# Performance work log

Measured on AMD Instinct MI355X. Metric: run time of the kernel, lower is better.

The kernel has to match this reference:

```python
import jax, jax.numpy as jnp
import numpy as np

N = 10000
E = 160000
IN_DIM = 256
PROJ_DIM = 512
HIDDEN = 512
OUT_DIM = 512
HEADS1, HEADS2, HEADS3 = 4, 4, 1
NEG_SLOPE = 0.2  # PyG GATConv default


def gat_conv(x, edge_index, W, att_src, att_dst, bias, heads, out_c, concat):
    """PyG GATConv (eval mode), with self-loops already appended to edge_index.
    x: [N, F_in]; W: [F_in, heads*out_c]; att_src/att_dst: [heads, out_c]; bias: [heads*out_c] or [out_c]."""
    n = x.shape[0]
    h = (x @ W).reshape(n, heads, out_c)            # [N, H, C]
    a_src = jnp.einsum('nhc,hc->nh', h, att_src)     # [N, H]
    a_dst = jnp.einsum('nhc,hc->nh', h, att_dst)     # [N, H]
    src, dst = edge_index[0], edge_index[1]
    e = jax.nn.leaky_relu(a_src[src] + a_dst[dst], NEG_SLOPE)  # [E, H]
    # segment softmax over incoming edges per destination node
    e_max = jax.ops.segment_max(e, dst, num_segments=n)
    e_exp = jnp.exp(e - e_max[dst])
    denom = jax.ops.segment_sum(e_exp, dst, num_segments=n)
    alpha = e_exp / denom[dst]                       # [E, H]
    msg = alpha[:, :, None] * h[src]                 # [E, H, C]
    out = jax.ops.segment_sum(msg, dst, num_segments=n)  # [N, H, C]
    out = out.reshape(n, heads * out_c) if concat else out.mean(axis=1)
    return out + bias


def setup_inputs() -> dict:
    key = jax.random.key(0)
    ks = jax.random.split(key, 16)
    g = 0.1
    inp = {
        'x': jax.random.normal(ks[0], (N, IN_DIM), dtype=jnp.float32),
        'edge_index': jax.random.randint(ks[1], (2, E), 0, N, dtype=jnp.int64),
        'proj_W': jax.random.normal(ks[2], (IN_DIM, PROJ_DIM), dtype=jnp.float32) * g,
        'proj_b': jnp.zeros((PROJ_DIM,), dtype=jnp.float32),
        'W1': jax.random.normal(ks[3], (PROJ_DIM, HEADS1 * HIDDEN), dtype=jnp.float32) * g,
        'as1': jax.random.normal(ks[4], (HEADS1, HIDDEN), dtype=jnp.float32) * g,
        'ad1': jax.random.normal(ks[5], (HEADS1, HIDDEN), dtype=jnp.float32) * g,
        'b1': jnp.zeros((HEADS1 * HIDDEN,), dtype=jnp.float32),
        'W2': jax.random.normal(ks[6], (HEADS1 * HIDDEN, HEADS2 * HIDDEN), dtype=jnp.float32) * g * 0.5,
        'as2': jax.random.normal(ks[7], (HEADS2, HIDDEN), dtype=jnp.float32) * g,
        'ad2': jax.random.normal(ks[8], (HEADS2, HIDDEN), dtype=jnp.float32) * g,
        'b2': jnp.zeros((HEADS2 * HIDDEN,), dtype=jnp.float32),
        'W3': jax.random.normal(ks[9], (HEADS2 * HIDDEN, HEADS3 * OUT_DIM), dtype=jnp.float32) * g * 0.5,
        'as3': jax.random.normal(ks[10], (HEADS3, OUT_DIM), dtype=jnp.float32) * g,
        'ad3': jax.random.normal(ks[11], (HEADS3, OUT_DIM), dtype=jnp.float32) * g,
        'b3': jnp.zeros((OUT_DIM,), dtype=jnp.float32),
    }
    return inp


def reference(x, edge_index, proj_W, proj_b, W1, as1, ad1, b1, W2, as2, ad2, b2, W3, as3, ad3, b3):
    # append self-loops once (PyG GATConv add_self_loops=True)
    loops = jnp.arange(N, dtype=edge_index.dtype)
    ei = jnp.concatenate([edge_index, jnp.stack([loops, loops])], axis=1)
    h = x @ proj_W + proj_b                                   # [N, 512]
    h = jax.nn.elu(gat_conv(h, ei, W1, as1, ad1, b1, HEADS1, HIDDEN, True))
    h = jax.nn.elu(gat_conv(h, ei, W2, as2, ad2, b2, HEADS2, HIDDEN, True))
    return gat_conv(h, ei, W3, as3, ad3, b3, HEADS3, OUT_DIM, False)  # [N, 512]
```

## Files before the change

### kernel.cpp

```cpp
#include <hip/hip_runtime.h>
#include <hip/hip_bf16.h>


#define LB(x) __launch_bounds__(x)

typedef unsigned short u16;
typedef unsigned int u32;
typedef __attribute__((ext_vector_type(8))) short short8;
typedef __attribute__((ext_vector_type(8))) short bf16x8;
typedef __attribute__((ext_vector_type(8))) _Float16 f16x8;
typedef __attribute__((ext_vector_type(4))) float f32x4;

__device__ __forceinline__ float b2f(u16 u) {
    union { float f; u32 u; } x;
    x.u = ((u32)u) << 16;
    return x.f;
}
__device__ __forceinline__ u16 f2b(float f) {
    u32 u = __float_as_uint(f);
    u = (u + 0x7FFFu + ((u >> 16) & 1u)) >> 16;
    return (u16)u;
}
__device__ __forceinline__ u16 f2h(float f) {
    union { _Float16 h; u16 u; } x;
    x.h = (_Float16)f;
    return x.u;
}
__device__ __forceinline__ float h2f(u16 u) {
    union { _Float16 h; u16 u; } x;
    x.u = u;
    return (float)x.h;
}
__device__ __forceinline__ void lds_cp16(const void* g, void* l) {
    __builtin_amdgcn_global_load_lds(
        (const __attribute__((address_space(1))) unsigned int*)g,
        (__attribute__((address_space(3))) unsigned int*)l, 16, 0, 0);
}

__global__ void k_deg(const int* __restrict__ ei, int E, int Np, int* __restrict__ deg) {
    int e = blockIdx.x * blockDim.x + threadIdx.x;
    if (e >= E + Np) return;
    int dst = (e < E) ? ei[E + e] : (e - E);
    atomicAdd(&deg[dst], 1);
}

__global__ LB(256) void k_s1(const int* __restrict__ deg, int* __restrict__ row_ptr,
                             int* __restrict__ bsum, int n) {
    __shared__ int sh[256];
    int b = blockIdx.x, t = threadIdx.x;
    int i = b * 256 + t;
    int v = (i < n) ? deg[i] : 0;
    sh[t] = v;
    __syncthreads();
    #pragma unroll
    for (int off = 1; off < 256; off <<= 1) {
        int add = (t >= off) ? sh[t - off] : 0;
        __syncthreads();
        sh[t] += add;
        __syncthreads();
    }
    if (i < n) row_ptr[i + 1] = sh[t];
    if (t == 255) bsum[b] = sh[255];
}

__global__ LB(64) void k_s2(int* __restrict__ bsum, int* __restrict__ boff, int nb) {
    __shared__ int sh[64];
    int t = threadIdx.x;
    sh[t] = (t < nb) ? bsum[t] : 0;
    __syncthreads();
    #pragma unroll
    for (int off = 1; off < 64; off <<= 1) {
        int add = (t >= off) ? sh[t - off] : 0;
        __syncthreads();
        sh[t] += add;
        __syncthreads();
    }
    if (t < nb) boff[t] = (t == 0) ? 0 : sh[t - 1];
}

__global__ LB(256) void k_s3(const int* __restrict__ deg, int* __restrict__ row_ptr,
                             const int* __restrict__ boff, int* __restrict__ cursor, int n) {
    int b = blockIdx.x, t = threadIdx.x;
    int i = b * 256 + t;
    if (i == 0) row_ptr[0] = 0;
    if (i < n) {
        int inc = row_ptr[i + 1] + boff[b];
        row_ptr[i + 1] = inc;
        cursor[i] = inc - deg[i];
    }
}

__global__ void k_fill(const int* __restrict__ ei, int E, int Np,
                       int* __restrict__ cursor, int* __restrict__ col_src) {
    int e = blockIdx.x * blockDim.x + threadIdx.x;
    if (e >= E + Np) return;
    int src, dst;
    if (e < E) { src = ei[e]; dst = ei[E + e]; }
    else       { src = dst = e - E; }
    int pos = atomicAdd(&cursor[dst], 1);
    col_src[pos] = src;
}

__global__ void k_pack(const float* __restrict__ in, u16* __restrict__ hi,
                       u16* __restrict__ lo, int n4) {
    int i = blockIdx.x * blockDim.x + threadIdx.x;
    if (i >= n4) return;
    float4 v = ((const float4*)in)[i];
    ushort4 h, l;
    h.x = f2b(v.x); l.x = f2b(v.x - b2f(h.x));
    h.y = f2b(v.y); l.y = f2b(v.y - b2f(h.y));
    h.z = f2b(v.z); l.z = f2b(v.z - b2f(h.z));
    h.w = f2b(v.w); l.w = f2b(v.w - b2f(h.w));
    ((ushort4*)hi)[i] = h;
    ((ushort4*)lo)[i] = l;
}

template<bool F16S>
__global__ LB(256) void k_wt_pack(const float* __restrict__ W, u16* __restrict__ Whi,
                                  u16* __restrict__ Wlo, int K, int Nn) {
    __shared__ float sh[32][33];
    int n0 = blockIdx.x * 32, k0 = blockIdx.y * 32;
    int c = threadIdx.x & 31, r0 = threadIdx.x >> 5;
    #pragma unroll
    for (int r = r0; r < 32; r += 8)
        sh[r][c] = W[(size_t)(k0 + r) * Nn + n0 + c];
    __syncthreads();
    #pragma unroll
    for (int r = r0; r < 32; r += 8) {
        float v = sh[c][r];
        if (F16S) {
            Whi[(size_t)(n0 + r) * K + k0 + c] = f2h(v);
        } else {
            u16 hi = f2b(v);
            Whi[(size_t)(n0 + r) * K + k0 + c] = hi;
            Wlo[(size_t)(n0 + r) * K + k0 + c] = f2b(v - b2f(hi));
        }
    }
}

__global__ LB(64) void k_bfold(const float* __restrict__ pb,
                               const u16* __restrict__ w1t_hi, const u16* __restrict__ w1t_lo,
                               float* __restrict__ bfold, int K) {
    int n = blockIdx.x;
    int lane = threadIdx.x;
    float s = 0.f;
    for (int k = lane; k < K; k += 64) {
        float w = b2f(w1t_hi[(size_t)n * K + k]) + b2f(w1t_lo[(size_t)n * K + k]);
        s = fmaf(pb[k], w, s);
    }
    #pragma unroll
    for (int off = 32; off; off >>= 1) s += __shfl_xor(s, off);
    if (lane == 0) bfold[n] = s;
}

template<int NFR, int PREC, int OUTMODE, bool ATT>
__global__ LB(256) void k_gemm_pl(const u16* __restrict__ Ahi, const u16* __restrict__ Alo,
                                  const u16* __restrict__ Bhi, const u16* __restrict__ Blo,
                                  const float* __restrict__ bias,
                                  u16* __restrict__ Chi, u16* __restrict__ Clo,
                                  u16* __restrict__ Cf16,
                                  const float* __restrict__ att_s, const float* __restrict__ att_d,
                                  float* __restrict__ a_src, float* __restrict__ a_dst,
                                  int HH, int M, int K, int Nn) {
    constexpr int BN = NFR * 32;
    constexpr int ALO_SZ = (PREC == 0) ? 128 * 32 : 8;
    constexpr int BLO_SZ = (PREC == 0) ? BN * 32 : 8;
    __shared__ u16 AsHi[128 * 32];
    __shared__ u16 AsLo[ALO_SZ];
    __shared__ u16 BsHi[BN * 32];
    __shared__ u16 BsLo[BLO_SZ];
    const int tid  = threadIdx.x;
    const int lane = tid & 63;
    const int w    = tid >> 6;
    const int wr   = w >> 1;
    const int wc   = w & 1;
    const int row0 = blockIdx.y * 128;
    const int col0 = blockIdx.x * BN;
    const int ln15 = lane & 15;
    const int lq   = lane >> 4;

    f32x4 acc[4][NFR];
    #pragma unroll
    for (int m = 0; m < 4; ++m)
        #pragma unroll
        for (int n = 0; n < NFR; ++n) acc[m][n] = (f32x4){0.f, 0.f, 0.f, 0.f};

    for (int k0 = 0; k0 < K; k0 += 32) {
        #pragma unroll
        for (int i = 0; i < 2; ++i) {
            int c = i * 256 + tid;
            int r  = 2 * (c >> 3) + (((c >> 2) ^ (c >> 4)) & 1);
            int kc = (c & 3) ^ (r & 3);
            int gra = row0 + r; if (gra >= M) gra = M - 1;
            size_t ga = (size_t)gra * K + k0 + kc * 8;
            lds_cp16(Ahi + ga, (char*)AsHi + c * 16);
            if (PREC == 0) lds_cp16(Alo + ga, (char*)AsLo + c * 16);
        }
        #pragma unroll
        for (int i = 0; i < NFR / 2; ++i) {
            int c = i * 256 + tid;
            int r  = 2 * (c >> 3) + (((c >> 2) ^ (c >> 4)) & 1);
            int kc = (c & 3) ^ (r & 3);
            size_t gb = (size_t)(col0 + r) * K + k0 + kc * 8;
            lds_cp16(Bhi + gb, (char*)BsHi + c * 16);
            if (PREC == 0) lds_cp16(Blo + gb, (char*)BsLo + c * 16);
        }
        __syncthreads();
        if (PREC == 0) {
            bf16x8 ah[4], al[4], bh[NFR], bl[NFR];
            #pragma unroll
            for (int m = 0; m < 4; ++m) {
                int row = wr * 64 + m * 16 + ln15;
                int byo = (row * 64 + lq * 16) ^ ((row & 7) << 4);
                ah[m] = *(const bf16x8*)((const char*)AsHi + byo);
                al[m] = *(const bf16x8*)((const char*)AsLo + byo);
            }
            #pragma unroll
            for (int n = 0; n < NFR; ++n) {
                int row = wc * (NFR * 16) + n * 16 + ln15;
                int byo = (row * 64 + lq * 16) ^ ((row & 7) << 4);
                bh[n] = *(const bf16x8*)((const char*)BsHi + byo);
                bl[n] = *(const bf16x8*)((const char*)BsLo + byo);
            }
            #pragma unroll
            for (int m = 0; m < 4; ++m)
                #pragma unroll
                for (int n = 0; n < NFR; ++n) {
                    acc[m][n] = __builtin_amdgcn_mfma_f32_16x16x32_bf16(al[m], bh[n], acc[m][n], 0, 0, 0);
                    acc[m][n] = __builtin_amdgcn_mfma_f32_16x16x32_bf16(ah[m], bl[n], acc[m][n], 0, 0, 0);
                    acc[m][n] = __builtin_amdgcn_mfma_f32_16x16x32_bf16(ah[m], bh[n], acc[m][n], 0, 0, 0);
                }
        } else {
            f16x8 a[4], b[NFR];
            #pragma unroll
            for (int m = 0; m < 4; ++m) {
                int row = wr * 64 + m * 16 + ln15;
                int byo = (row * 64 + lq * 16) ^ ((row & 7) << 4);
                a[m] = *(const f16x8*)((const char*)AsHi + byo);
            }
            #pragma unroll
            for (int n = 0; n < NFR; ++n) {
                int row = wc * (NFR * 16) + n * 16 + ln15;
                int byo = (row * 64 + lq * 16) ^ ((row & 7) << 4);
                b[n] = *(const f16x8*)((const char*)BsHi + byo);
            }
            #pragma unroll
            for (int m = 0; m < 4; ++m)
                #pragma unroll
                for (int n = 0; n < NFR; ++n)
                    acc[m][n] = __builtin_amdgcn_mfma_f32_16x16x32_f16(a[m], b[n], acc[m][n], 0, 0, 0);
        }
        __syncthreads();
    }

    #pragma unroll
    for (int m = 0; m < 4; ++m) {
        #pragma unroll
        for (int n = 0; n < NFR; ++n) {
            int gc = col0 + wc * (NFR * 16) + n * 16 + ln15;
            float badd = bias ? bias[gc] : 0.f;
            #pragma unroll
            for (int j = 0; j < 4; ++j) {
                int gr = row0 + wr * 64 + m * 16 + lq * 4 + j;
                if (gr < M) {
                    float v = acc[m][n][j] + badd;
                    size_t o = (size_t)gr * Nn + gc;
                    if (OUTMODE == 0) {
                        u16 hi = f2b(v);
                        Chi[o] = hi;
                        Clo[o] = f2b(v - b2f(hi));
                    } else {
                        Cf16[o] = f2h(v);
                    }
                }
            }
        }
    }

    if (ATT) {
        float atts[NFR], attd[NFR], bb[NFR];
        #pragma unroll
        for (int n = 0; n < NFR; ++n) {
            int gc = col0 + wc * (NFR * 16) + n * 16 + ln15;
            atts[n] = att_s[gc];
            attd[n] = att_d[gc];
            bb[n]   = bias ? bias[gc] : 0.f;
        }
        const int head = (col0 + wc * (NFR * 16)) >> 9;
        #pragma unroll
        for (int m = 0; m < 4; ++m) {
            #pragma unroll
            for (int j = 0; j < 4; ++j) {
                int gr = row0 + wr * 64 + m * 16 + lq * 4 + j;
                float s1 = 0.f, s2 = 0.f;
                #pragma unroll
                for (int n = 0; n < NFR; ++n) {
                    float v = acc[m][n][j] + bb[n];
                    s1 = fmaf(v, atts[n], s1);
                    s2 = fmaf(v, attd[n], s2);
                }
                #pragma unroll
                for (int off = 1; off < 16; off <<= 1) {
                    s1 += __shfl_xor(s1, off);
                    s2 += __shfl_xor(s2, off);
                }
                if (ln15 == 0 && gr < M) {
                    atomicAdd(&a_src[gr * HH + head], s1);
                    atomicAdd(&a_dst[gr * HH + head], s2);
                }
            }
        }
    }
}

template<int HH>
__global__ LB(64) void k_softmax(const int* __restrict__ row_ptr, const int* __restrict__ col_src,
                                 const float* __restrict__ a_src, const float* __restrict__ a_dst,
                                 float* __restrict__ alpha) {
    int d = blockIdx.x;
    int t = threadIdx.x;
    int s = row_ptr[d], eend = row_ptr[d + 1];
    int cnt = eend - s;
    float adh[HH];
    #pragma unroll
    for (int h = 0; h < HH; ++h) adh[h] = a_dst[d * HH + h];

    if (cnt <= 64) {
        bool act = t < cnt;
        float av[HH];
        #pragma unroll
        for (int h = 0; h < HH; ++h) av[h] = 0.f;
        if (act) {
            int src = col_src[s + t];
            if (HH == 4) {
                float4 q = ((const float4*)a_src)[src];
                av[0] = q.x; av[1] = q.y; av[2] = q.z; av[3] = q.w;
            } else {
                av[0] = a_src[src];
            }
        }
        float v[HH], m[HH], sum[HH];
        #pragma unroll
        for (int h = 0; h < HH; ++h) {
            float x = av[h] + adh[h];
            x = (x > 0.f) ? x : 0.2f * x;
            v[h] = act ? x : -1e30f;
            m[h] = v[h];
        }
        #pragma unroll
        for (int off = 32; off; off >>= 1)
            #pragma unroll
            for (int h = 0; h < HH; ++h) m[h] = fmaxf(m[h], __shfl_xor(m[h], off));
        #pragma unroll
        for (int h = 0; h < HH; ++h) {
            float e = act ? __expf(v[h] - m[h]) : 0.f;
            v[h] = e;
            sum[h] = e;
        }
        #pragma unroll
        for (int off = 32; off; off >>= 1)
            #pragma unroll
            for (int h = 0; h < HH; ++h) sum[h] += __shfl_xor(sum[h], off);
        if (act) {
            if (HH == 4) {
                float4 o;
                o.x = v[0] / sum[0]; o.y = v[1] / sum[1];
                o.z = v[2] / sum[2]; o.w = v[3] / sum[3];
                ((float4*)alpha)[s + t] = o;
            } else {
                alpha[s + t] = v[0] / sum[0];
            }
        }
        return;
    }

    for (int h = 0; h < HH; ++h) {
        float m = -1e30f;
        for (int e = s + t; e < eend; e += 64) {
            float x = a_src[col_src[e] * HH + h] + adh[h];
            x = (x > 0.f) ? x : 0.2f * x;
            m = fmaxf(m, x);
        }
        #pragma unroll
        for (int off = 32; off; off >>= 1) m = fmaxf(m, __shfl_xor(m, off));
        float sum = 0.f;
        for (int e = s + t; e < eend; e += 64) {
            float x = a_src[col_src[e] * HH + h] + adh[h];
            x = (x > 0.f) ? x : 0.2f * x;
            sum += __expf(x - m);
        }
        #pragma unroll
        for (int off = 32; off; off >>= 1) sum += __shfl_xor(sum, off);
        float inv = 1.0f / sum;
        for (int e = s + t; e < eend; e += 64) {
            float x = a_src[col_src[e] * HH + h] + adh[h];
            x = (x > 0.f) ? x : 0.2f * x;
            alpha[e * HH + h] = __expf(x - m) * inv;
        }
    }
}

template <int OMODE, bool ELU_>
__global__ LB(256) void k_agg(const int* __restrict__ row_ptr, const int* __restrict__ col_src,
                              const float* __restrict__ alpha, const u16* __restrict__ hf,
                              const float* __restrict__ bias,
                              u16* __restrict__ Oh, float* __restrict__ Of, int H, int C) {
    int d = blockIdx.x;
    int tid = threadIdx.x;
    int F = H * C;
    int o = tid * 8;
    int h0 = o / C;
    float acc[8];
    #pragma unroll
    for (int j = 0; j < 8; ++j) acc[j] = 0.f;
    int s = row_ptr[d], eend = row_ptr[d + 1];

    short8 v; float a;
    if (s < eend) {
        int src = col_src[s];
        a = alpha[s * H + h0];
        v = *(const short8*)(hf + (size_t)src * F + o);
    }
    for (int e = s; e < eend; ++e) {
        short8 w_; float an;
        bool more = (e + 1 < eend);
        if (more) {
            int srcn = col_src[e + 1];
            an = alpha[(e + 1) * H + h0];
            w_ = *(const short8*)(hf + (size_t)srcn * F + o);
        }
        #pragma unroll
        for (int j = 0; j < 8; ++j)
            acc[j] = fmaf(a, h2f((u16)v[j]), acc[j]);
        if (more) { a = an; v = w_; }
    }

    #pragma unroll
    for (int j = 0; j < 8; ++j) {
        acc[j] += bias[o + j];
        if (ELU_) acc[j] = (acc[j] > 0.f) ? acc[j] : __expf(acc[j]) - 1.f;
    }
    if (OMODE == 0) {
        short8 r;
        #pragma unroll
        for (int j = 0; j < 8; ++j) r[j] = (short)f2h(acc[j]);
        *(short8*)(Oh + (size_t)d * F + o) = r;
    } else {
        float* po = Of + (size_t)d * F + o;
        #pragma unroll
        for (int j4 = 0; j4 < 2; ++j4) {
            float4 r;
            r.x = acc[j4 * 4 + 0]; r.y = acc[j4 * 4 + 1];
            r.z = acc[j4 * 4 + 2]; r.w = acc[j4 * 4 + 3];
            *(float4*)&po[j4 * 4] = r;
        }
    }
}

extern "C" void kernel_launch(void* const* d_in, const int* in_sizes, int n_in,
                              void* d_out, int out_size, void* d_ws, size_t ws_size,
                              hipStream_t stream) {
    const float* x      = (const float*)d_in[0];
    const int*   ei     = (const int*)d_in[1];
    const float* proj_W = (const float*)d_in[2];
    const float* proj_b = (const float*)d_in[3];
    const float* W1  = (const float*)d_in[4];
    const float* as1 = (const float*)d_in[5];
    const float* ad1 = (const float*)d_in[6];
    const float* b1  = (const float*)d_in[7];
    const float* W2  = (const float*)d_in[8];
    const float* as2 = (const float*)d_in[9];
    const float* ad2 = (const float*)d_in[10];
    const float* b2  = (const float*)d_in[11];
    const float* W3  = (const float*)d_in[12];
    const float* as3 = (const float*)d_in[13];
    const float* ad3 = (const float*)d_in[14];
    const float* b3  = (const float*)d_in[15];

    const int N  = in_sizes[0] / 256;
    const int E  = in_sizes[1] / 2;
    const int Ep = E + N;
    const int NB = (N + 255) / 256;

    size_t off = 0;
    auto alloc = [&](size_t bytes) -> void* {
        void* p = (char*)d_ws + off;
        off += (bytes + 255) & ~(size_t)255;
        return p;
    };
    u16* bufX    = (u16*)alloc((size_t)N * 2048 * 2);
    u16* bufY    = (u16*)alloc((size_t)N * 2048 * 2);
    u16* xb_hi   = (u16*)alloc((size_t)N * 256 * 2);
    u16* xb_lo   = (u16*)alloc((size_t)N * 256 * 2);
    u16* pw_hi   = (u16*)alloc((size_t)256 * 512 * 2);
    u16* pw_lo   = (u16*)alloc((size_t)256 * 512 * 2);
    u16* wf_hi   = (u16*)alloc((size_t)2048 * 256 * 2);
    u16* wf_lo   = (u16*)alloc((size_t)2048 * 256 * 2);
    float* bfold   = (float*)alloc((size_t)2048 * 4);
    float* att_z   = (float*)alloc((size_t)N * 18 * 4);
    float* alpha   = (float*)alloc((size_t)Ep * 4 * 4);
    int*   deg     = (int*)alloc((size_t)N * 4);
    int*   cursor  = (int*)alloc((size_t)N * 4);
    int*   row_ptr = (int*)alloc((size_t)(N + 1) * 4);
    int*   col_src = (int*)alloc((size_t)Ep * 4);
    int*   bsum    = (int*)alloc((size_t)NB * 4);
    int*   boff    = (int*)alloc((size_t)NB * 4);
    (void)ws_size;

    float* a_src1 = att_z;
    float* a_dst1 = att_z + (size_t)N * 4;
    float* a_src2 = att_z + (size_t)N * 8;
    float* a_dst2 = att_z + (size_t)N * 12;
    float* a_src3 = att_z + (size_t)N * 16;
    float* a_dst3 = att_z + (size_t)N * 17;

    u16* whi = (u16*)d_out;
    u16* wlo = (u16*)d_out + (size_t)2048 * 2048;

    hipMemsetAsync(deg, 0, (size_t)N * 4, stream);
    hipMemsetAsync(att_z, 0, (size_t)N * 18 * 4, stream);
    int eb = (Ep + 255) / 256;
    k_deg<<<eb, 256, 0, stream>>>(ei, E, N, deg);
    k_s1<<<NB, 256, 0, stream>>>(deg, row_ptr, bsum, N);
    k_s2<<<1, 64, 0, stream>>>(bsum, boff, NB);
    k_s3<<<NB, 256, 0, stream>>>(deg, row_ptr, boff, cursor, N);
    k_fill<<<eb, 256, 0, stream>>>(ei, E, N, cursor, col_src);

    const int MB1 = (N + 127) / 128;

    k_pack<<<(N * 256 / 4 + 255) / 256, 256, 0, stream>>>(x, xb_hi, xb_lo, N * 256 / 4);
    k_pack<<<(256 * 512 / 4 + 255) / 256, 256, 0, stream>>>(proj_W, pw_hi, pw_lo, 256 * 512 / 4);

    k_wt_pack<false><<<dim3(2048 / 32, 512 / 32), 256, 0, stream>>>(W1, whi, wlo, 512, 2048);
    k_bfold<<<2048, 64, 0, stream>>>(proj_b, whi, wlo, bfold, 512);
    k_gemm_pl<2, 0, 0, false><<<dim3(256 / 64, 2048 / 128), 256, 0, stream>>>(
        whi, wlo, pw_hi, pw_lo, nullptr, wf_hi, wf_lo, nullptr,
        nullptr, nullptr, nullptr, nullptr, 0, 2048, 512, 256);

    k_gemm_pl<4, 0, 2, true><<<dim3(2048 / 128, MB1), 256, 0, stream>>>(
        xb_hi, xb_lo, wf_hi, wf_lo, bfold, nullptr, nullptr, bufX,
        as1, ad1, a_src1, a_dst1, 4, N, 256, 2048);
    k_softmax<4><<<N, 64, 0, stream>>>(row_ptr, col_src, a_src1, a_dst1, alpha);
    k_agg<0, true><<<N, 256, 0, stream>>>(row_ptr, col_src, alpha, bufX,
                                          b1, bufY, nullptr, 4, 512);

    k_wt_pack<true><<<dim3(2048 / 32, 2048 / 32), 256, 0, stream>>>(W2, whi, nullptr, 2048, 2048);
    k_gemm_pl<4, 2, 2, true><<<dim3(2048 / 128, MB1), 256, 0, stream>>>(
        bufY, nullptr, whi, nullptr, nullptr, nullptr, nullptr, bufX,
        as2, ad2, a_src2, a_dst2, 4, N, 2048, 2048);
    k_softmax<4><<<N, 64, 0, stream>>>(row_ptr, col_src, a_src2, a_dst2, alpha);
    k_agg<0, true><<<N, 256, 0, stream>>>(row_ptr, col_src, alpha, bufX,
                                          b2, bufY, nullptr, 4, 512);

    k_wt_pack<true><<<dim3(512 / 32, 2048 / 32), 256, 0, stream>>>(W3, whi, nullptr, 2048, 512);
    k_gemm_pl<2, 2, 2, true><<<dim3(512 / 64, MB1), 256, 0, stream>>>(
        bufY, nullptr, whi, nullptr, nullptr, nullptr, nullptr, bufX,
        as3, ad3, a_src3, a_dst3, 1, N, 2048, 512);
    k_softmax<1><<<N, 64, 0, stream>>>(row_ptr, col_src, a_src3, a_dst3, alpha);
    k_agg<1, false><<<N, 64, 0, stream>>>(row_ptr, col_src, alpha, bufX,
                                          b3, nullptr, (float*)d_out, 1, 512);
}
```

Before: 638.0 us.

## Fuse segment softmax into aggregation and widen layer-2 GEMM tile to 256 rows

Merges the per-destination softmax kernel into the aggregation kernel. Each wavefront now computes attention weights for its own head into shared memory and consumes them directly, so the alpha buffer and one launch per layer go away. The GEMM is templated on warp rows so the large layer-2 GEMM can use 512-thread, 256-row tiles to improve B-tile reuse. Risks are extra block syncs in the high-degree path, a larger LDS footprint, and a loader indexing scheme that must still cover the larger tiles correctly.

```diff
diff --git a/kernel.cpp b/kernel.cpp
--- a/kernel.cpp
+++ b/kernel.cpp
@@ -153,19 +153,23 @@
     if (lane == 0) bfold[n] = s;
 }
 
-template<int NFR, int PREC, int OUTMODE, bool ATT>
-__global__ LB(256) void k_gemm_pl(const u16* __restrict__ Ahi, const u16* __restrict__ Alo,
-                                  const u16* __restrict__ Bhi, const u16* __restrict__ Blo,
-                                  const float* __restrict__ bias,
-                                  u16* __restrict__ Chi, u16* __restrict__ Clo,
-                                  u16* __restrict__ Cf16,
-                                  const float* __restrict__ att_s, const float* __restrict__ att_d,
-                                  float* __restrict__ a_src, float* __restrict__ a_dst,
-                                  int HH, int M, int K, int Nn) {
+template<int WM, int NFR, int PREC, int OUTMODE, bool ATT>
+__global__ __launch_bounds__(WM * 128)
+void k_gemm_pl(const u16* __restrict__ Ahi, const u16* __restrict__ Alo,
+               const u16* __restrict__ Bhi, const u16* __restrict__ Blo,
+               const float* __restrict__ bias,
+               u16* __restrict__ Chi, u16* __restrict__ Clo,
+               u16* __restrict__ Cf16,
+               const float* __restrict__ att_s, const float* __restrict__ att_d,
+               float* __restrict__ a_src, float* __restrict__ a_dst,
+               int HH, int M, int K, int Nn) {
+    constexpr int BM = WM * 64;
     constexpr int BN = NFR * 32;
-    constexpr int ALO_SZ = (PREC == 0) ? 128 * 32 : 8;
+    constexpr int T  = WM * 128;
+    constexpr int BITER = (NFR * 128) / T > 0 ? (NFR * 128) / T : 1;
+    constexpr int ALO_SZ = (PREC == 0) ? BM * 32 : 8;
     constexpr int BLO_SZ = (PREC == 0) ? BN * 32 : 8;
-    __shared__ u16 AsHi[128 * 32];
+    __shared__ u16 AsHi[BM * 32];
     __shared__ u16 AsLo[ALO_SZ];
     __shared__ u16 BsHi[BN * 32];
     __shared__ u16 BsLo[BLO_SZ];
@@ -174,7 +178,7 @@
     const int w    = tid >> 6;
     const int wr   = w >> 1;
     const int wc   = w & 1;
-    const int row0 = blockIdx.y * 128;
+    const int row0 = blockIdx.y * BM;
     const int col0 = blockIdx.x * BN;
     const int ln15 = lane & 15;
     const int lq   = lane >> 4;
@@ -188,7 +192,7 @@
     for (int k0 = 0; k0 < K; k0 += 32) {
         #pragma unroll
         for (int i = 0; i < 2; ++i) {
-            int c = i * 256 + tid;
+            int c = i * T + tid;
             int r  = 2 * (c >> 3) + (((c >> 2) ^ (c >> 4)) & 1);
             int kc = (c & 3) ^ (r & 3);
             int gra = row0 + r; if (gra >= M) gra = M - 1;
@@ -197,8 +201,8 @@
             if (PREC == 0) lds_cp16(Alo + ga, (char*)AsLo + c * 16);
         }
         #pragma unroll
-        for (int i = 0; i < NFR / 2; ++i) {
-            int c = i * 256 + tid;
+        for (int i = 0; i < BITER; ++i) {
+            int c = i * T + tid;
             int r  = 2 * (c >> 3) + (((c >> 2) ^ (c >> 4)) & 1);
             int kc = (c & 3) ^ (r & 3);
             size_t gb = (size_t)(col0 + r) * K + k0 + kc * 8;
@@ -313,126 +317,101 @@
     }
 }
 
-template<int HH>
-__global__ LB(64) void k_softmax(const int* __restrict__ row_ptr, const int* __restrict__ col_src,
-                                 const float* __restrict__ a_src, const float* __restrict__ a_dst,
-                                 float* __restrict__ alpha) {
-    int d = blockIdx.x;
-    int t = threadIdx.x;
-    int s = row_ptr[d], eend = row_ptr[d + 1];
-    int cnt = eend - s;
-    float adh[HH];
-    #pragma unroll
-    for (int h = 0; h < HH; ++h) adh[h] = a_dst[d * HH + h];
+template <int HH, int OMODE, bool ELU_>
+__global__ __launch_bounds__(HH * 64)
+void k_sagg(const int* __restrict__ row_ptr, const int* __restrict__ col_src,
+            const float* __restrict__ a_src, const float* __restrict__ a_dst,
+            const u16* __restrict__ hf, const float* __restrict__ bias,
+            u16* __restrict__ Oh, float* __restrict__ Of, int C) {
+    __shared__ float sal[HH * 64];
+    const int d    = blockIdx.x;
+    const int tid  = threadIdx.x;
+    const int w    = tid >> 6;
+    const int lane = tid & 63;
+    const int F    = HH * C;
+    const int o    = tid * 8;
+    const int s = row_ptr[d], eend = row_ptr[d + 1];
+    const int cnt = eend - s;
+    const float adh = a_dst[d * HH + w];
+
+    float acc[8];
+    #pragma unroll
+    for (int j = 0; j < 8; ++j) acc[j] = 0.f;
 
     if (cnt <= 64) {
-        bool act = t < cnt;
-        float av[HH];
-        #pragma unroll
-        for (int h = 0; h < HH; ++h) av[h] = 0.f;
-        if (act) {
-            int src = col_src[s + t];
-            if (HH == 4) {
-                float4 q = ((const float4*)a_src)[src];
-                av[0] = q.x; av[1] = q.y; av[2] = q.z; av[3] = q.w;
-            } else {
-                av[0] = a_src[src];
-            }
-        }
-        float v[HH], m[HH], sum[HH];
-        #pragma unroll
-        for (int h = 0; h < HH; ++h) {
-            float x = av[h] + adh[h];
-            x = (x > 0.f) ? x : 0.2f * x;
-            v[h] = act ? x : -1e30f;
-            m[h] = v[h];
-        }
-        #pragma unroll
-        for (int off = 32; off; off >>= 1)
-            #pragma unroll
-            for (int h = 0; h < HH; ++h) m[h] = fmaxf(m[h], __shfl_xor(m[h], off));
-        #pragma unroll
-        for (int h = 0; h < HH; ++h) {
-            float e = act ? __expf(v[h] - m[h]) : 0.f;
-            v[h] = e;
-            sum[h] = e;
-        }
-        #pragma unroll
-        for (int off = 32; off; off >>= 1)
-            #pragma unroll
-            for (int h = 0; h < HH; ++h) sum[h] += __shfl_xor(sum[h], off);
-        if (act) {
-            if (HH == 4) {
-                float4 o;
-                o.x = v[0] / sum[0]; o.y = v[1] / sum[1];
-                o.z = v[2] / sum[2]; o.w = v[3] / sum[3];
-                ((float4*)alpha)[s + t] = o;
-            } else {
-                alpha[s + t] = v[0] / sum[0];
-            }
-        }
-        return;
-    }
-
-    for (int h = 0; h < HH; ++h) {
+        bool act = lane < cnt;
+        float av = act ? a_src[col_src[s + lane] * HH + w] : 0.f;
+        float x = av + adh;
+        x = (x > 0.f) ? x : 0.2f * x;
+        float v = act ? x : -1e30f;
+        float m = v;
+        #pragma unroll
+        for (int off = 32; off; off >>= 1) m = fmaxf(m, __shfl_xor(m, off));
+        float e_ = act ? __expf(v - m) : 0.f;
+        float sum = e_;
+        #pragma unroll
+        for (int off = 32; off; off >>= 1) sum += __shfl_xor(sum, off);
+        if (act) sal[w * 64 + lane] = e_ / sum;
+        __syncthreads();
+
+        if (cnt > 0) {
+            short8 vv; float a;
+            {
+                int src0 = col_src[s];
+                a = sal[w * 64];
+                vv = *(const short8*)(hf + (size_t)src0 * F + o);
+            }
+            for (int i = 0; i < cnt; ++i) {
+                short8 w_; float an;
+                bool more = (i + 1 < cnt);
+                if (more) {
+                    int srcn = col_src[s + i + 1];
+                    an = sal[w * 64 + i + 1];
+                    w_ = *(const short8*)(hf + (size_t)srcn * F + o);
+                }
+                #pragma unroll
+                for (int j = 0; j < 8; ++j)
+                    acc[j] = fmaf(a, h2f((u16)vv[j]), acc[j]);
+                if (more) { a = an; vv = w_; }
+            }
+        }
+    } else {
         float m = -1e30f;
-        for (int e = s + t; e < eend; e += 64) {
-            float x = a_src[col_src[e] * HH + h] + adh[h];
+        for (int e = s + lane; e < eend; e += 64) {
+            float x = a_src[col_src[e] * HH + w] + adh;
             x = (x > 0.f) ? x : 0.2f * x;
             m = fmaxf(m, x);
         }
         #pragma unroll
         for (int off = 32; off; off >>= 1) m = fmaxf(m, __shfl_xor(m, off));
         float sum = 0.f;
-        for (int e = s + t; e < eend; e += 64) {
-            float x = a_src[col_src[e] * HH + h] + adh[h];
+        for (int e = s + lane; e < eend; e += 64) {
+            float x = a_src[col_src[e] * HH + w] + adh;
             x = (x > 0.f) ? x : 0.2f * x;
             sum += __expf(x - m);
         }
         #pragma unroll
         for (int off = 32; off; off >>= 1) sum += __shfl_xor(sum, off);
         float inv = 1.0f / sum;
-        for (int e = s + t; e < eend; e += 64) {
-            float x = a_src[col_src[e] * HH + h] + adh[h];
-            x = (x > 0.f) ? x : 0.2f * x;
-            alpha[e * HH + h] = __expf(x - m) * inv;
-        }
-    }
-}
-
-template <int OMODE, bool ELU_>
-__global__ LB(256) void k_agg(const int* __restrict__ row_ptr, const int* __restrict__ col_src,
-                              const float* __restrict__ alpha, const u16* __restrict__ hf,
-                              const float* __restrict__ bias,
-                              u16* __restrict__ Oh, float* __restrict__ Of, int H, int C) {
-    int d = blockIdx.x;
-    int tid = threadIdx.x;
-    int F = H * C;
-    int o = tid * 8;
-    int h0 = o / C;
-    float acc[8];
-    #pragma unroll
-    for (int j = 0; j < 8; ++j) acc[j] = 0.f;
-    int s = row_ptr[d], eend = row_ptr[d + 1];
-
-    short8 v; float a;
-    if (s < eend) {
-        int src = col_src[s];
-        a = alpha[s * H + h0];
-        v = *(const short8*)(hf + (size_t)src * F + o);
-    }
-    for (int e = s; e < eend; ++e) {
-        short8 w_; float an;
-        bool more = (e + 1 < eend);
-        if (more) {
-            int srcn = col_src[e + 1];
-            an = alpha[(e + 1) * H + h0];
-            w_ = *(const short8*)(hf + (size_t)srcn * F + o);
-        }
-        #pragma unroll
-        for (int j = 0; j < 8; ++j)
-            acc[j] = fmaf(a, h2f((u16)v[j]), acc[j]);
-        if (more) { a = an; v = w_; }
+        for (int base = s; base < eend; base += 64) {
+            int e = base + lane;
+            if (e < eend) {
+                float x = a_src[col_src[e] * HH + w] + adh;
+                x = (x > 0.f) ? x : 0.2f * x;
+                sal[w * 64 + lane] = __expf(x - m) * inv;
+            }
+            __syncthreads();
+            int nn = (eend - base < 64) ? (eend - base) : 64;
+            for (int i = 0; i < nn; ++i) {
+                int src = col_src[base + i];
+                float a = sal[w * 64 + i];
+                short8 vv = *(const short8*)(hf + (size_t)src * F + o);
+                #pragma unroll
+                for (int j = 0; j < 8; ++j)
+                    acc[j] = fmaf(a, h2f((u16)vv[j]), acc[j]);
+            }
+            __syncthreads();
+        }
     }
 
     #pragma unroll
@@ -498,7 +477,6 @@
     u16* wf_lo   = (u16*)alloc((size_t)2048 * 256 * 2);
     float* bfold   = (float*)alloc((size_t)2048 * 4);
     float* att_z   = (float*)alloc((size_t)N * 18 * 4);
-    float* alpha   = (float*)alloc((size_t)Ep * 4 * 4);
     int*   deg     = (int*)alloc((size_t)N * 4);
     int*   cursor  = (int*)alloc((size_t)N * 4);
     int*   row_ptr = (int*)alloc((size_t)(N + 1) * 4);
@@ -527,36 +505,34 @@
     k_fill<<<eb, 256, 0, stream>>>(ei, E, N, cursor, col_src);
 
     const int MB1 = (N + 127) / 128;
+    const int MB2 = (N + 255) / 256;
 
     k_pack<<<(N * 256 / 4 + 255) / 256, 256, 0, stream>>>(x, xb_hi, xb_lo, N * 256 / 4);
     k_pack<<<(256 * 512 / 4 + 255) / 256, 256, 0, stream>>>(proj_W, pw_hi, pw_lo, 256 * 512 / 4);
 
     k_wt_pack<false><<<dim3(2048 / 32, 512 / 32), 256, 0, stream>>>(W1, whi, wlo, 512, 2048);
     k_bfold<<<2048, 64, 0, stream>>>(proj_b, whi, wlo, bfold, 512);
-    k_gemm_pl<2, 0, 0, false><<<dim3(256 / 64, 2048 / 128), 256, 0, stream>>>(
+    k_gemm_pl<2, 2, 0, 0, false><<<dim3(256 / 64, 2048 / 128), 256, 0, stream>>>(
         whi, wlo, pw_hi, pw_lo, nullptr, wf_hi, wf_lo, nullptr,
         nullptr, nullptr, nullptr, nullptr, 0, 2048, 512, 256);
 
-    k_gemm_pl<4, 0, 2, true><<<dim3(2048 / 128, MB1), 256, 0, stream>>>(
+    k_gemm_pl<2, 4, 0, 2, true><<<dim3(2048 / 128, MB1), 256, 0, stream>>>(
         xb_hi, xb_lo, wf_hi, wf_lo, bfold, nullptr, nullptr, bufX,
         as1, ad1, a_src1, a_dst1, 4, N, 256, 2048);
-    k_softmax<4><<<N, 64, 0, stream>>>(row_ptr, col_src, a_src1, a_dst1, alpha);
-    k_agg<0, true><<<N, 256, 0, stream>>>(row_ptr, col_src, alpha, bufX,
-                                          b1, bufY, nullptr, 4, 512);
+    k_sagg<4, 0, true><<<N, 256, 0, stream>>>(row_ptr, col_src, a_src1, a_dst1,
+                                              bufX, b1, bufY, nullptr, 512);
 
     k_wt_pack<true><<<dim3(2048 / 32, 2048 / 32), 256, 0, stream>>>(W2, whi, nullptr, 2048, 2048);
-    k_gemm_pl<4, 2, 2, true><<<dim3(2048 / 128, MB1), 256, 0, stream>>>(
+    k_gemm_pl<4, 4, 2, 2, true><<<dim3(2048 / 128, MB2), 512, 0, stream>>>(
         bufY, nullptr, whi, nullptr, nullptr, nullptr, nullptr, bufX,
         as2, ad2, a_src2, a_dst2, 4, N, 2048, 2048);
-    k_softmax<4><<<N, 64, 0, stream>>>(row_ptr, col_src, a_src2, a_dst2, alpha);
-    k_agg<0, true><<<N, 256, 0, stream>>>(row_ptr, col_src, alpha, bufX,
-                                          b2, bufY, nullptr, 4, 512);
+    k_sagg<4, 0, true><<<N, 256, 0, stream>>>(row_ptr, col_src, a_src2, a_dst2,
+                                              bufX, b2, bufY, nullptr, 512);
 
     k_wt_pack<true><<<dim3(512 / 32, 2048 / 32), 256, 0, stream>>>(W3, whi, nullptr, 2048, 512);
-    k_gemm_pl<2, 2, 2, true><<<dim3(512 / 64, MB1), 256, 0, stream>>>(
+    k_gemm_pl<2, 2, 2, 2, true><<<dim3(512 / 64, MB1), 256, 0, stream>>>(
         bufY, nullptr, whi, nullptr, nullptr, nullptr, nullptr, bufX,
         as3, ad3, a_src3, a_dst3, 1, N, 2048, 512);
-    k_softmax<1><<<N, 64, 0, stream>>>(row_ptr, col_src, a_src3, a_dst3, alpha);
-    k_agg<1, false><<<N, 64, 0, stream>>>(row_ptr, col_src, alpha, bufX,
-                                          b3, nullptr, (float*)d_out, 1, 512);
-}
+    k_sagg<1, 1, false><<<N, 64, 0, stream>>>(row_ptr, col_src, a_src3, a_dst3,
+                                              bufX, b3, nullptr, (float*)d_out, 512);
+}
```

New measurement: 623.8 us. -2.2%, faster.
